# Kernel optimization log

Hardware: AMD Instinct MI355X
Metric: run time of the kernel (lower is better)

The kernel has to match this reference:

```python
import jax, jax.numpy as jnp
import numpy as np

# parameter limits (low, high) as in Filter_param.limits
LIMITS = {
    'f_start': (200.0, 4000.0),
    'f_inf': (20.0, 500.0),
    'f_decay': (0.0, 2.0),
    'f_T': (0.0, 2.0),
    'w_offset': (0.0, 1.0),
    'w_T': (0.01, 0.5),
}

B, T = 2048, 8192

def setup_inputs() -> dict:
    key = jax.random.key(0)
    ks = jax.random.split(key, 7)
    return {
        'X': jax.random.normal(ks[0], (B, T), dtype=jnp.float32),
        'F': 44100,  # sampling frequency (int constant)
        'f_start_normal': jax.random.normal(ks[1], (), dtype=jnp.float32),
        'f_inf_normal': jax.random.normal(ks[2], (), dtype=jnp.float32),
        'f_decay_normal': jax.random.normal(ks[3], (), dtype=jnp.float32),
        'f_T_normal': jax.random.normal(ks[4], (), dtype=jnp.float32),
        'w_offset_normal': jax.random.normal(ks[5], (), dtype=jnp.float32),
        'w_T_normal': jax.random.normal(ks[6], (), dtype=jnp.float32),
    }

def _squash(v, name):
    low, high = LIMITS[name]
    return low + (high - low) * jax.nn.sigmoid(v)

def reference(X, F, f_start_normal, f_inf_normal, f_decay_normal,
              f_T_normal, w_offset_normal, w_T_normal):
    Bsz, Tlen = X.shape
    c = (2.0 ** (1.0 / 3.0) - 1.0) ** 0.5 * F / np.pi  # scalar cutoff constant
    t = jnp.arange(Tlen, dtype=X.dtype) / Tlen  # normalized time [T]

    f_start = _squash(f_start_normal, 'f_start')
    f_inf = _squash(f_inf_normal, 'f_inf')
    f_decay = _squash(f_decay_normal, 'f_decay')
    f_T = _squash(f_T_normal, 'f_T')
    w_offset = _squash(w_offset_normal, 'w_offset')
    w_T = _squash(w_T_normal, 'w_T')

    # time-varying cutoff frequency and output window
    f = f_inf + (f_start - f_inf) * (0.7 * 0.1 ** f_decay) ** (t / (10.0 * 0.1 ** f_T))  # [T]
    w = jax.nn.sigmoid((t - w_offset) / w_T)  # [T]
    a = (f - c) / (f + c)  # [T]
    b = (a + 1.0) / 2.0    # [T]

    # cascaded time-varying one-pole recurrence (two stages), scanned over time.
    # t=0: y1 = y2 = X[:,0];   t>0:
    #   y1[t] = b[t]*(x[t] + x[t-1]) - a[t]*y1[t-1]
    #   y2[t] = b[t]*(y1[t] + y1[t-1]) - a[t]*y2[t-1]
    x0 = X[:, 0]
    init = (x0, x0, x0, w[0] * x0)  # (y0_prev, y1_prev, y2_prev, acc)

    def step(carry, inp):
        y0p, y1p, y2p, acc = carry
        x_t, a_t, b_t, w_t = inp
        y1 = b_t * (x_t + y0p) - a_t * y1p
        y2 = b_t * (y1 + y1p) - a_t * y2p
        return (x_t, y1, y2, acc + w_t * y2), None

    xs = (X[:, 1:].T, a[1:], b[1:], w[1:])  # time-major [T-1, ...]
    (_, _, _, acc), _ = jax.lax.scan(step, init, xs)

    return acc / jnp.sum(w)  # prediction [B]
```

## Files before the change

### kernel.cpp

```cpp
#include <hip/hip_runtime.h>
#include <math.h>

#define BB 2048
#define TT 8192
#define CC 128
#define LL 64

#define OFF_A4    132096
#define OFF_WSUM  134144
#define OFF_Q     135168

__device__ inline float sigmoid_dev(float v) {
    return 1.0f / (1.0f + expf(-v));
}

__device__ inline float squash_dev(float v, float lo, float hi) {
    return lo + (hi - lo) * sigmoid_dev(v);
}

struct SquashedParams {
    float c, f_start, f_inf, log2K_invTd, w_offset, w_T;
};

__device__ inline SquashedParams load_params(const int* Fp,
                                             const float* p_fstart, const float* p_finf,
                                             const float* p_fdecay, const float* p_fT,
                                             const float* p_woff, const float* p_wT) {
    SquashedParams P;
    float Fv       = (float)(*Fp);
    P.c            = sqrtf(exp2f(1.0f / 3.0f) - 1.0f) * Fv / 3.14159265358979323846f;
    P.f_start      = squash_dev(*p_fstart, 200.0f, 4000.0f);
    P.f_inf        = squash_dev(*p_finf,   20.0f,  500.0f);
    float f_decay  = squash_dev(*p_fdecay, 0.0f,   2.0f);
    float f_T      = squash_dev(*p_fT,     0.0f,   2.0f);
    P.w_offset     = squash_dev(*p_woff,   0.0f,   1.0f);
    P.w_T          = squash_dev(*p_wT,     0.01f,  0.5f);
    const float LOG2_10 = 3.32192809488736235f;
    float log2K  = log2f(0.7f) - LOG2_10 * f_decay;
    float invTd  = 0.1f * exp2f(LOG2_10 * f_T);
    P.log2K_invTd = log2K * invTd;
    return P;
}

__global__ void coef_kernel(const int* Fp,
                            const float* p_fstart, const float* p_finf,
                            const float* p_fdecay, const float* p_fT,
                            const float* p_woff, const float* p_wT,
                            float4* __restrict__ coef) {
    int t = blockIdx.x * blockDim.x + threadIdx.x;
    if (t >= TT + LL) return;
    float4 cf;
    if (t >= TT) {
        cf = make_float4(0.0f, 0.0f, 0.0f, 0.0f);
    } else {
        SquashedParams P = load_params(Fp, p_fstart, p_finf, p_fdecay, p_fT, p_woff, p_wT);
        float ti = (float)t * (1.0f / (float)TT);
        float f  = P.f_inf + (P.f_start - P.f_inf) * exp2f(P.log2K_invTd * ti);
        float a  = (f - P.c) / (f + P.c);
        float b  = 0.5f * (a + 1.0f);
        float m  = -a;
        float p  = b * (1.0f + m);
        float z  = (ti - P.w_offset) / P.w_T;
        z        = fminf(fmaxf(z, -60.0f), 60.0f);
        float w  = 1.0f / (1.0f + expf(-z));
        cf = make_float4(m, b, p, w);
    }
    coef[t] = cf;
}

__global__ void chunkmat_kernel(const float4* __restrict__ coef,
                                float4* __restrict__ A4, float* __restrict__ Wsum) {
    int j = threadIdx.x;
    if (j >= CC) return;
    const float4* cf = coef + 1 + j * LL;
    float al = 1.0f, be = 0.0f, ga = 0.0f, de = 0.0f, ws = 0.0f;
    #pragma unroll 8
    for (int k = 0; k < LL; k++) {
        float4 c4 = cf[k];
        float m = c4.x, p = c4.z, w = c4.w;
        float nal = m * al;
        float nbe = fmaf(p, al, m * be);
        de = fmaf(w * m, al, de);
        ga = fmaf(w, nbe, ga);
        al = nal; be = nbe;
        ws += w;
    }
    A4[j] = make_float4(al, be, ga, de);
    Wsum[j] = ws;
}

__global__ void chunk_kernel(const float* __restrict__ X, const float4* __restrict__ coef,
                             float* __restrict__ Q1, float* __restrict__ Q2,
                             float* __restrict__ Q3) {
    int j = blockIdx.x >> 3;
    int b = ((blockIdx.x & 7) << 8) + threadIdx.x;

    __shared__ float4 sc[LL];
    if (threadIdx.x < LL) sc[threadIdx.x] = coef[1 + j * LL + threadIdx.x];
    __syncthreads();

    const float* base = X + (size_t)b * TT + j * LL;
    float e[LL];
    #pragma unroll
    for (int i = 0; i < LL / 4; i++) {
        float4 v = reinterpret_cast<const float4*>(base)[i];
        e[4 * i + 0] = v.x; e[4 * i + 1] = v.y;
        e[4 * i + 2] = v.z; e[4 * i + 3] = v.w;
    }
    float e_next = (j < CC - 1) ? base[LL] : 0.0f;

    float y1 = 0.0f, y2 = 0.0f, acc = 0.0f;
    #pragma unroll
    for (int k = 0; k < LL; k++) {
        float4 c4 = sc[k];
        float x  = (k < LL - 1) ? e[k + 1] : e_next;
        float xp = e[k];
        float u  = c4.y * (x + xp);
        float y2n = fmaf(c4.x, y2, fmaf(c4.z, y1, c4.y * u));
        y1 = fmaf(c4.x, y1, u);
        y2 = y2n;
        acc = fmaf(c4.w, y2n, acc);
    }
    int idx = j * BB + b;
    Q1[idx] = y1; Q2[idx] = y2; Q3[idx] = acc;
}

__global__ void combine_kernel(const float* __restrict__ X, const float4* __restrict__ coef,
                               const float4* __restrict__ A4, const float* __restrict__ Wsum,
                               const float* __restrict__ Q1, const float* __restrict__ Q2,
                               const float* __restrict__ Q3, float* __restrict__ out) {
    int b = blockIdx.x * blockDim.x + threadIdx.x;
    float x0 = X[(size_t)b * TT];
    float w0 = coef[0].w;
    float y1 = x0, y2 = x0, acc = w0 * x0, sumw = w0;
    for (int j = 0; j < CC; j++) {
        float4 A = A4[j];
        int idx = j * BB + b;
        float q1 = Q1[idx], q2 = Q2[idx], q3 = Q3[idx];
        float ny1 = fmaf(A.x, y1, q1);
        float ny2 = fmaf(A.x, y2, fmaf(A.y, y1, q2));
        acc += fmaf(A.z, y1, fmaf(A.w, y2, q3));
        sumw += Wsum[j];
        y1 = ny1; y2 = ny2;
    }
    out[b] = acc / sumw;
}

extern "C" void kernel_launch(void* const* d_in, const int* in_sizes, int n_in,
                              void* d_out, int out_size, void* d_ws, size_t ws_size,
                              hipStream_t stream) {
    const float* X        = (const float*)d_in[0];
    const int*   Fp       = (const int*)d_in[1];
    const float* p_fstart = (const float*)d_in[2];
    const float* p_finf   = (const float*)d_in[3];
    const float* p_fdecay = (const float*)d_in[4];
    const float* p_fT     = (const float*)d_in[5];
    const float* p_woff   = (const float*)d_in[6];
    const float* p_wT     = (const float*)d_in[7];
    float* out = (float*)d_out;

    char* ws = (char*)d_ws;
    float4* coef = (float4*)ws;
    float4* A4   = (float4*)(ws + OFF_A4);
    float*  Wsum = (float*)(ws + OFF_WSUM);
    float*  Q1   = (float*)(ws + OFF_Q);
    float*  Q2   = Q1 + CC * BB;
    float*  Q3   = Q2 + CC * BB;

    coef_kernel<<<(TT + LL + 255) / 256, 256, 0, stream>>>(
        Fp, p_fstart, p_finf, p_fdecay, p_fT, p_woff, p_wT, coef);
    chunkmat_kernel<<<1, CC, 0, stream>>>(coef, A4, Wsum);
    chunk_kernel<<<CC * 8, 256, 0, stream>>>(X, coef, Q1, Q2, Q3);
    combine_kernel<<<BB / 256, 256, 0, stream>>>(X, coef, A4, Wsum, Q1, Q2, Q3, out);
}
```

Before: 131.7 us.

## Fuse coefficient setup, pack chunk states, and parallelize chunk combine via wave scan

Removes the separate coefficient kernel by recomputing step coefficients on the fly in the setup and chunk kernels. Chunk states are packed into one float4 store per element. The combine stage, which walked 128 chunks serially per row, now uses one wavefront per row with a shuffle-based tree composition of the affine chunk transforms. This cuts launch count and the serial combine latency, at the cost of redundant transcendental math per block and more shuffles.

Measured after the change: 124.7 us. -5.3%, faster.

```diff
diff --git a/kernel.cpp b/kernel.cpp
--- a/kernel.cpp
+++ b/kernel.cpp
@@ -6,20 +6,16 @@
 #define CC 128
 #define LL 64
 
-#define OFF_A4    132096
-#define OFF_WSUM  134144
-#define OFF_Q     135168
-
-__device__ inline float sigmoid_dev(float v) {
-    return 1.0f / (1.0f + expf(-v));
-}
-
+#define OFF_SC  2048
+#define OFF_Q   4096
+
+__device__ inline float sigmoid_dev(float v) { return 1.0f / (1.0f + expf(-v)); }
 __device__ inline float squash_dev(float v, float lo, float hi) {
     return lo + (hi - lo) * sigmoid_dev(v);
 }
 
 struct SquashedParams {
-    float c, f_start, f_inf, log2K_invTd, w_offset, w_T;
+    float c, f_start, f_inf, log2K_invTd, w_offset, inv_w_T;
 };
 
 __device__ inline SquashedParams load_params(const int* Fp,
@@ -27,14 +23,15 @@
                                              const float* p_fdecay, const float* p_fT,
                                              const float* p_woff, const float* p_wT) {
     SquashedParams P;
-    float Fv       = (float)(*Fp);
-    P.c            = sqrtf(exp2f(1.0f / 3.0f) - 1.0f) * Fv / 3.14159265358979323846f;
-    P.f_start      = squash_dev(*p_fstart, 200.0f, 4000.0f);
-    P.f_inf        = squash_dev(*p_finf,   20.0f,  500.0f);
-    float f_decay  = squash_dev(*p_fdecay, 0.0f,   2.0f);
-    float f_T      = squash_dev(*p_fT,     0.0f,   2.0f);
-    P.w_offset     = squash_dev(*p_woff,   0.0f,   1.0f);
-    P.w_T          = squash_dev(*p_wT,     0.01f,  0.5f);
+    float Fv      = (float)(*Fp);
+    P.c           = sqrtf(exp2f(1.0f / 3.0f) - 1.0f) * Fv / 3.14159265358979323846f;
+    P.f_start     = squash_dev(*p_fstart, 200.0f, 4000.0f);
+    P.f_inf       = squash_dev(*p_finf,   20.0f,  500.0f);
+    float f_decay = squash_dev(*p_fdecay, 0.0f,   2.0f);
+    float f_T     = squash_dev(*p_fT,     0.0f,   2.0f);
+    P.w_offset    = squash_dev(*p_woff,   0.0f,   1.0f);
+    float w_T     = squash_dev(*p_wT,     0.01f,  0.5f);
+    P.inv_w_T     = 1.0f / w_T;
     const float LOG2_10 = 3.32192809488736235f;
     float log2K  = log2f(0.7f) - LOG2_10 * f_decay;
     float invTd  = 0.1f * exp2f(LOG2_10 * f_T);
@@ -42,41 +39,28 @@
     return P;
 }
 
-__global__ void coef_kernel(const int* Fp,
-                            const float* p_fstart, const float* p_finf,
-                            const float* p_fdecay, const float* p_fT,
-                            const float* p_woff, const float* p_wT,
-                            float4* __restrict__ coef) {
-    int t = blockIdx.x * blockDim.x + threadIdx.x;
-    if (t >= TT + LL) return;
-    float4 cf;
-    if (t >= TT) {
-        cf = make_float4(0.0f, 0.0f, 0.0f, 0.0f);
-    } else {
-        SquashedParams P = load_params(Fp, p_fstart, p_finf, p_fdecay, p_fT, p_woff, p_wT);
-        float ti = (float)t * (1.0f / (float)TT);
-        float f  = P.f_inf + (P.f_start - P.f_inf) * exp2f(P.log2K_invTd * ti);
-        float a  = (f - P.c) / (f + P.c);
-        float b  = 0.5f * (a + 1.0f);
-        float m  = -a;
-        float p  = b * (1.0f + m);
-        float z  = (ti - P.w_offset) / P.w_T;
-        z        = fminf(fmaxf(z, -60.0f), 60.0f);
-        float w  = 1.0f / (1.0f + expf(-z));
-        cf = make_float4(m, b, p, w);
-    }
-    coef[t] = cf;
-}
-
-__global__ void chunkmat_kernel(const float4* __restrict__ coef,
-                                float4* __restrict__ A4, float* __restrict__ Wsum) {
+__device__ inline float4 step_coef(const SquashedParams& P, int tg) {
+    if (tg >= TT - 1) return make_float4(0.0f, 0.0f, 0.0f, 0.0f);
+    float ti = (float)(tg + 1) * (1.0f / (float)TT);
+    float f  = P.f_inf + (P.f_start - P.f_inf) * exp2f(P.log2K_invTd * ti);
+    float a  = (f - P.c) / (f + P.c);
+    float b  = 0.5f * (a + 1.0f);
+    float m  = -a;
+    float p  = b * (1.0f + m);
+    float w  = sigmoid_dev((ti - P.w_offset) * P.inv_w_T);
+    return make_float4(m, b, p, w);
+}
+
+__global__ void setup_kernel(const int* Fp,
+                             const float* p_fstart, const float* p_finf,
+                             const float* p_fdecay, const float* p_fT,
+                             const float* p_woff, const float* p_wT,
+                             float4* __restrict__ A4, float* __restrict__ SC) {
     int j = threadIdx.x;
-    if (j >= CC) return;
-    const float4* cf = coef + 1 + j * LL;
+    SquashedParams P = load_params(Fp, p_fstart, p_finf, p_fdecay, p_fT, p_woff, p_wT);
     float al = 1.0f, be = 0.0f, ga = 0.0f, de = 0.0f, ws = 0.0f;
-    #pragma unroll 8
     for (int k = 0; k < LL; k++) {
-        float4 c4 = cf[k];
+        float4 c4 = step_coef(P, j * LL + k);
         float m = c4.x, p = c4.z, w = c4.w;
         float nal = m * al;
         float nbe = fmaf(p, al, m * be);
@@ -86,17 +70,36 @@
         ws += w;
     }
     A4[j] = make_float4(al, be, ga, de);
-    Wsum[j] = ws;
-}
-
-__global__ void chunk_kernel(const float* __restrict__ X, const float4* __restrict__ coef,
-                             float* __restrict__ Q1, float* __restrict__ Q2,
-                             float* __restrict__ Q3) {
+
+    __shared__ float sws[CC];
+    sws[j] = ws;
+    __syncthreads();
+    for (int s = CC / 2; s > 0; s >>= 1) {
+        if (j < s) sws[j] += sws[j + s];
+        __syncthreads();
+    }
+    if (j == 0) {
+        float w0 = sigmoid_dev((0.0f - P.w_offset) * P.inv_w_T);
+        float tot = w0 + sws[0];
+        SC[0] = 1.0f / tot;
+        SC[1] = w0;
+    }
+}
+
+__global__ void chunk_kernel(const float* __restrict__ X,
+                             const int* Fp,
+                             const float* p_fstart, const float* p_finf,
+                             const float* p_fdecay, const float* p_fT,
+                             const float* p_woff, const float* p_wT,
+                             float4* __restrict__ Q4) {
     int j = blockIdx.x >> 3;
     int b = ((blockIdx.x & 7) << 8) + threadIdx.x;
 
     __shared__ float4 sc[LL];
-    if (threadIdx.x < LL) sc[threadIdx.x] = coef[1 + j * LL + threadIdx.x];
+    if (threadIdx.x < LL) {
+        SquashedParams P = load_params(Fp, p_fstart, p_finf, p_fdecay, p_fT, p_woff, p_wT);
+        sc[threadIdx.x] = step_coef(P, j * LL + threadIdx.x);
+    }
     __syncthreads();
 
     const float* base = X + (size_t)b * TT + j * LL;
@@ -121,29 +124,54 @@
         y2 = y2n;
         acc = fmaf(c4.w, y2n, acc);
     }
-    int idx = j * BB + b;
-    Q1[idx] = y1; Q2[idx] = y2; Q3[idx] = acc;
-}
-
-__global__ void combine_kernel(const float* __restrict__ X, const float4* __restrict__ coef,
-                               const float4* __restrict__ A4, const float* __restrict__ Wsum,
-                               const float* __restrict__ Q1, const float* __restrict__ Q2,
-                               const float* __restrict__ Q3, float* __restrict__ out) {
-    int b = blockIdx.x * blockDim.x + threadIdx.x;
-    float x0 = X[(size_t)b * TT];
-    float w0 = coef[0].w;
-    float y1 = x0, y2 = x0, acc = w0 * x0, sumw = w0;
-    for (int j = 0; j < CC; j++) {
-        float4 A = A4[j];
-        int idx = j * BB + b;
-        float q1 = Q1[idx], q2 = Q2[idx], q3 = Q3[idx];
-        float ny1 = fmaf(A.x, y1, q1);
-        float ny2 = fmaf(A.x, y2, fmaf(A.y, y1, q2));
-        acc += fmaf(A.z, y1, fmaf(A.w, y2, q3));
-        sumw += Wsum[j];
-        y1 = ny1; y2 = ny2;
-    }
-    out[b] = acc / sumw;
+    Q4[j * BB + b] = make_float4(y1, y2, acc, 0.0f);
+}
+
+__global__ void combine_kernel(const float* __restrict__ X,
+                               const float4* __restrict__ A4, const float* __restrict__ SC,
+                               const float4* __restrict__ Q4, float* __restrict__ out) {
+    int wid  = threadIdx.x >> 6;
+    int lane = threadIdx.x & 63;
+    int r    = (blockIdx.x << 2) + wid;
+    int c0   = lane << 1;
+
+    float x0 = X[(size_t)r * TT];
+    float4 Aa = A4[c0], Ab = A4[c0 + 1];
+    float4 qa = Q4[(size_t)c0 * BB + r];
+    float4 qb = Q4[(size_t)(c0 + 1) * BB + r];
+
+    float al = Ab.x * Aa.x;
+    float be = fmaf(Ab.y, Aa.x, Ab.x * Aa.y);
+    float ga = fmaf(Ab.z, Aa.x, fmaf(Ab.w, Aa.y, Aa.z));
+    float de = fmaf(Ab.w, Aa.x, Aa.w);
+    float q1 = fmaf(Ab.x, qa.x, qb.x);
+    float q2 = fmaf(Ab.y, qa.x, fmaf(Ab.x, qa.y, qb.y));
+    float q3 = fmaf(Ab.z, qa.x, fmaf(Ab.w, qa.y, qa.z + qb.z));
+
+    #pragma unroll
+    for (int o = 1; o < 64; o <<= 1) {
+        float al2 = __shfl_down(al, o);
+        float be2 = __shfl_down(be, o);
+        float ga2 = __shfl_down(ga, o);
+        float de2 = __shfl_down(de, o);
+        float q12 = __shfl_down(q1, o);
+        float q22 = __shfl_down(q2, o);
+        float q32 = __shfl_down(q3, o);
+        float nal = al2 * al;
+        float nbe = fmaf(be2, al, al2 * be);
+        float nga = fmaf(ga2, al, fmaf(de2, be, ga));
+        float nde = fmaf(de2, al, de);
+        float nq1 = fmaf(al2, q1, q12);
+        float nq2 = fmaf(be2, q1, fmaf(al2, q2, q22));
+        float nq3 = fmaf(ga2, q1, fmaf(de2, q2, q3 + q32));
+        al = nal; be = nbe; ga = nga; de = nde; q1 = nq1; q2 = nq2; q3 = nq3;
+    }
+
+    if (lane == 0) {
+        float w0 = SC[1];
+        float accf = fmaf(ga + de + w0, x0, q3);
+        out[r] = accf * SC[0];
+    }
 }
 
 extern "C" void kernel_launch(void* const* d_in, const int* in_sizes, int n_in,
@@ -160,16 +188,13 @@
     float* out = (float*)d_out;
 
     char* ws = (char*)d_ws;
-    float4* coef = (float4*)ws;
-    float4* A4   = (float4*)(ws + OFF_A4);
-    float*  Wsum = (float*)(ws + OFF_WSUM);
-    float*  Q1   = (float*)(ws + OFF_Q);
-    float*  Q2   = Q1 + CC * BB;
-    float*  Q3   = Q2 + CC * BB;
-
-    coef_kernel<<<(TT + LL + 255) / 256, 256, 0, stream>>>(
-        Fp, p_fstart, p_finf, p_fdecay, p_fT, p_woff, p_wT, coef);
-    chunkmat_kernel<<<1, CC, 0, stream>>>(coef, A4, Wsum);
-    chunk_kernel<<<CC * 8, 256, 0, stream>>>(X, coef, Q1, Q2, Q3);
-    combine_kernel<<<BB / 256, 256, 0, stream>>>(X, coef, A4, Wsum, Q1, Q2, Q3, out);
-}
+    float4* A4 = (float4*)ws;
+    float*  SC = (float*)(ws + OFF_SC);
+    float4* Q4 = (float4*)(ws + OFF_Q);
+
+    setup_kernel<<<1, CC, 0, stream>>>(Fp, p_fstart, p_finf, p_fdecay, p_fT,
+                                       p_woff, p_wT, A4, SC);
+    chunk_kernel<<<CC * 8, 256, 0, stream>>>(X, Fp, p_fstart, p_finf, p_fdecay,
+                                             p_fT, p_woff, p_wT, Q4);
+    combine_kernel<<<BB / 4, 256, 0, stream>>>(X, A4, SC, Q4, out);
+}
```
